# Kernel optimization log

Measured on AMD Instinct MI355X. Metric: run time of the kernel, lower is better.

Reference implementation:

```python
import jax, jax.numpy as jnp
import numpy as np

# ---- fan-beam CT geometry (hard-coded in fidelity_module) ----
N = 256                      # image is N x N on [-20, 20]^2
A = 20                       # number of projection angles over [0, 2pi)
UDET = 624                   # detector pixels on [-60, 60]
S = 768                      # ray samples for line-integral quadrature
R_SRC = 59.0                 # source-to-origin radius
R_DET = 49.0                 # detector-to-origin radius
D_SD = R_SRC + R_DET         # source-to-detector distance
XMIN, XMAX = -20.0, 20.0
DX = (XMAX - XMIN) / N
UMIN, UMAX = -60.0, 60.0
DU = (UMAX - UMIN) / UDET
THETAS = ((np.arange(A) + 0.5) * 2.0 * np.pi / A).astype(np.float32)   # cell midpoints (odl.uniform_partition)
UCENT = (UMIN + (np.arange(UDET) + 0.5) * DU).astype(np.float32)       # detector cell midpoints
NFFT = 2048                  # FFT length for ramp filtering (>= 2*UDET)


def _bilinear(img, gx, gy):
    """img: [B,N,N] (axis0=x, axis1=y). gx, gy: fractional index coords, shape [...].
    Returns [B, ...] with zero outside the image."""
    i0 = jnp.floor(gx)
    j0 = jnp.floor(gy)
    fx = (gx - i0).astype(img.dtype)
    fy = (gy - j0).astype(img.dtype)
    i0 = i0.astype(jnp.int32)
    j0 = j0.astype(jnp.int32)

    def corner(ii, jj):
        valid = (ii >= 0) & (ii < N) & (jj >= 0) & (jj < N)
        v = img[:, jnp.clip(ii, 0, N - 1), jnp.clip(jj, 0, N - 1)]
        return jnp.where(valid[None], v, 0.0)

    return (corner(i0, j0) * (1 - fx) * (1 - fy)
            + corner(i0 + 1, j0) * fx * (1 - fy)
            + corner(i0, j0 + 1) * (1 - fx) * fy
            + corner(i0 + 1, j0 + 1) * fx * fy)


def forward_project(img):
    """Ray-driven fan-beam forward projection (Radon transform). img: [B,N,N] -> sino [B,A,UDET]."""
    cs = jnp.cos(jnp.asarray(THETAS))
    sn = jnp.sin(jnp.asarray(THETAS))
    src = R_SRC * jnp.stack([cs, sn], axis=-1)            # (A,2) source positions
    det_c = -R_DET * jnp.stack([cs, sn], axis=-1)         # (A,2) detector centers
    ddir = jnp.stack([-sn, cs], axis=-1)                  # (A,2) detector axis
    u = jnp.asarray(UCENT)
    p = det_c[:, None, :] + u[None, :, None] * ddir[:, None, :]   # (A,U,2) detector pixel positions
    ray = p - src[:, None, :]                             # (A,U,2)
    length = jnp.sqrt(jnp.sum(ray * ray, axis=-1))        # (A,U) ray length
    tt = (jnp.arange(S, dtype=jnp.float32) + 0.5) / S     # (S,) midpoint quadrature
    pts = src[:, None, None, :] + tt[None, None, :, None] * ray[:, :, None, :]  # (A,U,S,2)
    gx = (pts[..., 0] - XMIN) / DX - 0.5                  # fractional index along axis0 (x)
    gy = (pts[..., 1] - XMIN) / DX - 0.5                  # fractional index along axis1 (y)
    vals = _bilinear(img, gx, gy)                         # (B,A,U,S)
    return jnp.sum(vals, axis=-1) * (length / S)[None]    # (B,A,U)


def fbp(sino):
    """Filtered back-projection with Hann-windowed ramp filter (frequency_scaling=1).
    sino: [B,A,UDET] -> image [B,N,N]."""
    u = jnp.asarray(UCENT)
    # cosine pre-weighting for flat fan-beam detector
    g = sino * (D_SD / jnp.sqrt(D_SD * D_SD + u * u))[None, None, :]
    freqs = jnp.fft.rfftfreq(NFFT, d=DU).astype(jnp.float32)
    nyq = 1.0 / (2.0 * DU)
    ramp = jnp.abs(freqs)
    hann = 0.5 * (1.0 + jnp.cos(np.float32(np.pi) * freqs / nyq)) * (freqs <= nyq)
    filt = ramp * hann
    q = jnp.fft.irfft(jnp.fft.rfft(g, n=NFFT, axis=-1) * filt[None, None, :], n=NFFT, axis=-1)
    q = q[..., :UDET] * DU                                # (B,A,U) filtered sinogram

    cs = jnp.cos(jnp.asarray(THETAS))
    sn = jnp.sin(jnp.asarray(THETAS))
    xs = XMIN + (jnp.arange(N, dtype=jnp.float32) + 0.5) * DX
    X = xs[:, None]                                       # axis0 = x
    Y = xs[None, :]                                       # axis1 = y
    # distance from source plane to pixel along central ray: in [R_SRC-28, R_SRC+28], never ~0
    tdist = R_SRC - (X[None] * cs[:, None, None] + Y[None] * sn[:, None, None])   # (A,N,N)
    uu = D_SD * (-X[None] * sn[:, None, None] + Y[None] * cs[:, None, None]) / tdist  # detector coord of pixel
    k = (uu - UCENT[0]) / DU                              # fractional detector index (A,N,N)
    k0 = jnp.floor(k)
    fk = (k - k0).astype(sino.dtype)
    k0 = k0.astype(jnp.int32)
    aidx = jnp.arange(A)[:, None, None]

    def gather(kk):
        valid = (kk >= 0) & (kk < UDET)
        v = q[:, aidx, jnp.clip(kk, 0, UDET - 1)]         # (B,A,N,N)
        return jnp.where(valid[None], v, 0.0)

    val = gather(k0) * (1 - fk)[None] + gather(k0 + 1) * fk[None]
    w = (R_SRC / tdist) ** 2                              # fan-beam distance weighting
    dtheta = 2.0 * np.pi / A
    return 0.5 * np.float32(dtheta) * jnp.sum(w[None] * val, axis=1)  # (B,N,N)


def setup_inputs() -> dict:
    key = jax.random.key(0)
    k1, k2 = jax.random.split(key)
    input_data = jax.random.uniform(k1, (4, N, N), dtype=jnp.float32)
    proj = jax.random.normal(k2, (4, A, UDET), dtype=jnp.float32)
    return {"input_data": input_data, "proj": proj}


def reference(input_data, proj):
    # fidelity_module.forward: x_error = FBP(proj - Radon(input_data))
    p_tmp = forward_project(input_data)
    y_error = proj - p_tmp
    return fbp(y_error)
```

## Files before the change

### kernel.cpp

```cpp
#include <hip/hip_runtime.h>
#include <math.h>

#define NN 256
#define AA 20
#define UD 624
#define SS 768
#define NAU (AA*UD)
#define PI_D 3.14159265358979323846

__global__ __launch_bounds__(256) void k_prep(const float* __restrict__ img,
                                              float4* __restrict__ pixA,
                                              float4* __restrict__ pixB,
                                              float* __restrict__ hh) {
    __shared__ double red[256];
    const int blk = blockIdx.x;
    const int tid = threadIdx.x;
    if (blk < 256) {
        int idx = blk * 256 + tid;
        float4 v;
        v.x = img[idx];
        v.y = img[65536 + idx];
        v.z = img[131072 + idx];
        v.w = img[196608 + idx];
        pixA[idx] = v;
    } else if (blk < 512) {
        int oidx = (blk - 256) * 256 + tid;
        int j = oidx >> 8, i = oidx & 255;
        int idx = i * 256 + j;
        float4 v;
        v.x = img[idx];
        v.y = img[65536 + idx];
        v.z = img[131072 + idx];
        v.w = img[196608 + idx];
        pixB[oidx] = v;
    } else {
        const int n = blk - 512;
        double acc = 0.0;
        for (int k = 1 + tid; k < 1024; k += 256) {
            float a1 = 1.0f + cosf((float)PI_D * (float)k * (1.0f/1024.0f));
            int m = (k * n) & 2047;
            float c2 = cosf((float)PI_D * (float)m * (1.0f/1024.0f));
            acc += (double)((float)k * a1 * c2);
        }
        red[tid] = acc;
        __syncthreads();
        for (int s = 128; s > 0; s >>= 1) {
            if (tid < s) red[tid] += red[tid + s];
            __syncthreads();
        }
        if (tid == 0) hh[n] = (float)(red[0] * (1.0 / (2048.0 * 2048.0)));
    }
}

__global__ __launch_bounds__(256) void k_forward(const float4* __restrict__ pixA,
                                                 const float4* __restrict__ pixB,
                                                 const float* __restrict__ proj,
                                                 float* __restrict__ g) {
    const int wid = threadIdx.x >> 6;
    const int lane = threadIdx.x & 63;
    const int ray = blockIdx.x * 4 + wid;
    const int a = ray / UD;
    const int u = ray - a * UD;

    const float theta = (float)(((double)a + 0.5) * (2.0 * PI_D / (double)AA));
    float sn, cs;
    sincosf(theta, &sn, &cs);
    const float uc = (float)(-60.0 + ((double)u + 0.5) * (120.0 / 624.0));

    const float sx = 59.0f * cs, sy = 59.0f * sn;
    const float rx = -108.0f * cs - uc * sn;
    const float ry = -108.0f * sn + uc * cs;
    const float length = sqrtf(rx * rx + ry * ry);

    const float stepx = rx * (6.4f / 768.0f);
    const float basex = (sx + rx * (0.5f / 768.0f) + 20.0f) * 6.4f - 0.5f;
    const float stepy = ry * (6.4f / 768.0f);
    const float basey = (sy + ry * (0.5f / 768.0f) + 20.0f) * 6.4f - 0.5f;

    const bool useB = fabsf(stepx) > fabsf(stepy);
    const float4* __restrict__ im = useB ? pixB : pixA;
    const float bi = useB ? basex : basey;
    const float si = useB ? stepx : stepy;
    const float bo = useB ? basey : basex;
    const float so = useB ? stepy : stepx;

    float ax = 0.f, ay = 0.f, az = 0.f, aw = 0.f;

    for (int s = lane; s < SS; s += 64) {
        float gi = fmaf((float)s, si, bi);
        float go = fmaf((float)s, so, bo);
        float fgi = floorf(gi), fgo = floorf(go);
        float fi = gi - fgi, fo = go - fgo;
        int i0 = (int)fgi, o0 = (int)fgo;
        int i1 = i0 + 1, o1 = o0 + 1;
        float wi0 = (i0 >= 0 && i0 < NN) ? (1.0f - fi) : 0.0f;
        float wi1 = (i1 >= 0 && i1 < NN) ? fi : 0.0f;
        float wo0 = (o0 >= 0 && o0 < NN) ? (1.0f - fo) : 0.0f;
        float wo1 = (o1 >= 0 && o1 < NN) ? fo : 0.0f;
        int ic0 = min(max(i0, 0), NN - 1), ic1 = min(max(i1, 0), NN - 1);
        int oc0 = min(max(o0, 0), NN - 1), oc1 = min(max(o1, 0), NN - 1);
        const float4 c00 = im[oc0 * NN + ic0];
        const float4 c10 = im[oc0 * NN + ic1];
        const float4 c01 = im[oc1 * NN + ic0];
        const float4 c11 = im[oc1 * NN + ic1];
        float w00 = wi0 * wo0, w10 = wi1 * wo0, w01 = wi0 * wo1, w11 = wi1 * wo1;
        ax += w00 * c00.x + w10 * c10.x + w01 * c01.x + w11 * c11.x;
        ay += w00 * c00.y + w10 * c10.y + w01 * c01.y + w11 * c11.y;
        az += w00 * c00.z + w10 * c10.z + w01 * c01.z + w11 * c11.z;
        aw += w00 * c00.w + w10 * c10.w + w01 * c01.w + w11 * c11.w;
    }

    for (int off = 32; off > 0; off >>= 1) {
        ax += __shfl_down(ax, off);
        ay += __shfl_down(ay, off);
        az += __shfl_down(az, off);
        aw += __shfl_down(aw, off);
    }

    if (lane == 0) {
        const float scale = length * (1.0f / 768.0f);
        const float wdet = 108.0f / sqrtf(108.0f * 108.0f + uc * uc);
        g[0 * NAU + ray] = (proj[0 * NAU + ray] - ax * scale) * wdet;
        g[1 * NAU + ray] = (proj[1 * NAU + ray] - ay * scale) * wdet;
        g[2 * NAU + ray] = (proj[2 * NAU + ray] - az * scale) * wdet;
        g[3 * NAU + ray] = (proj[3 * NAU + ray] - aw * scale) * wdet;
    }
}

__global__ __launch_bounds__(128) void k_conv(const float* __restrict__ g,
                                              const float* __restrict__ hh,
                                              float* __restrict__ q) {
    __shared__ float sgp[752];
    const int row = blockIdx.x / 5;
    const int tile = blockIdx.x % 5;
    const int tid = threadIdx.x;

    for (int k = tid; k < 752; k += 128) {
        sgp[k] = (k >= 64 && k < 64 + UD) ? g[row * UD + (k - 64)] : 0.0f;
    }
    __syncthreads();

    const int j = tile * 128 + tid;
    const int jc = min(j, UD - 1);
    int wbase = tile * 128 + (tid & 64);
    wbase = __builtin_amdgcn_readfirstlane(wbase);
    const int tmax1 = min(wbase + 63, UD - 1);
    const int tmax2 = UD - 1 - wbase;

    float acc = 0.0f;
    for (int t = 0; t <= tmax1; ++t)
        acc += hh[t] * sgp[64 + jc - t];
    for (int t = 1; t <= tmax2; ++t)
        acc += hh[t] * sgp[64 + jc + t];

    if (j < UD) q[row * UD + j] = acc;
}

__global__ __launch_bounds__(256) void k_bp(const float* __restrict__ q,
                                            float* __restrict__ out) {
    __shared__ float scs[AA], ssn[AA];
    const int tid = threadIdx.x;
    if (tid < AA) {
        float th = (float)(((double)tid + 0.5) * (2.0 * PI_D / (double)AA));
        float s, c;
        sincosf(th, &s, &c);
        scs[tid] = c;
        ssn[tid] = s;
    }
    __syncthreads();

    const int p = blockIdx.x * 256 + tid;
    const int b = p >> 16;
    const int rem = p & 65535;
    const int i = rem >> 8;
    const int j = rem & 255;

    const float X = -20.0f + ((float)i + 0.5f) * 0.15625f;
    const float Y = -20.0f + ((float)j + 0.5f) * 0.15625f;

    const float uc0 = (float)(-60.0 + 0.5 * (120.0 / 624.0));
    const float duf = (float)(120.0 / 624.0);

    const float* __restrict__ qb = q + b * AA * UD;
    float acc = 0.0f;
#pragma unroll
    for (int a = 0; a < AA; ++a) {
        float cs = scs[a], sn = ssn[a];
        float t = 59.0f - (X * cs + Y * sn);
        float uu = 108.0f * (Y * cs - X * sn) / t;
        float k = (uu - uc0) / duf;
        float fk0 = floorf(k);
        float fk = k - fk0;
        int ik = (int)fk0;
        const float* qr = qb + a * UD;
        float v0 = ((unsigned)ik < (unsigned)UD) ? qr[ik] : 0.0f;
        float v1 = ((unsigned)(ik + 1) < (unsigned)UD) ? qr[ik + 1] : 0.0f;
        float val = v0 * (1.0f - fk) + v1 * fk;
        float w = 59.0f / t;
        acc += w * w * val;
    }
    out[p] = (0.5f * (float)(2.0 * PI_D / (double)AA)) * acc;
}

extern "C" void kernel_launch(void* const* d_in, const int* in_sizes, int n_in,
                              void* d_out, int out_size, void* d_ws, size_t ws_size,
                              hipStream_t stream) {
    const float* img  = (const float*)d_in[0];
    const float* proj = (const float*)d_in[1];
    float* out = (float*)d_out;

    char* ws = (char*)d_ws;
    float4* pixA = (float4*)ws;
    float4* pixB = (float4*)(ws + (1 << 20));
    float*  g    = (float*)(ws + (2 << 20));
    float*  q    = (float*)(ws + (2 << 20) + 199680);
    float*  hh   = (float*)(ws + (2 << 20) + 2 * 199680);

    k_prep<<<1136, 256, 0, stream>>>(img, pixA, pixB, hh);
    k_forward<<<NAU / 4, 256, 0, stream>>>(pixA, pixB, proj, g);
    k_conv<<<80 * 5, 128, 0, stream>>>(g, hh, q);
    k_bp<<<1024, 256, 0, stream>>>(q, out);
}
```

Baseline: 114.3 us.

## Pack four rays per wavefront in forward projection and split conv taps across waves

The forward projector now gives each wavefront four adjacent detector rays, with 16 lanes per ray looping over 48 sample steps. This cuts the grid to 780 blocks and shortens the shuffle reduction. Adjacent rays sample nearby pixels, which should improve cache locality. The convolution kernel now spreads each output's tap range over four waves of 256 threads and sums the partials through shared memory, which raises parallelism for the long serial dot products.

After: 116.1 us. No clear change (+1.6%).

```diff
diff --git a/kernel.cpp b/kernel.cpp
--- a/kernel.cpp
+++ b/kernel.cpp
@@ -18,20 +18,14 @@
     if (blk < 256) {
         int idx = blk * 256 + tid;
         float4 v;
-        v.x = img[idx];
-        v.y = img[65536 + idx];
-        v.z = img[131072 + idx];
-        v.w = img[196608 + idx];
+        v.x = img[idx]; v.y = img[65536 + idx]; v.z = img[131072 + idx]; v.w = img[196608 + idx];
         pixA[idx] = v;
     } else if (blk < 512) {
         int oidx = (blk - 256) * 256 + tid;
         int j = oidx >> 8, i = oidx & 255;
         int idx = i * 256 + j;
         float4 v;
-        v.x = img[idx];
-        v.y = img[65536 + idx];
-        v.z = img[131072 + idx];
-        v.w = img[196608 + idx];
+        v.x = img[idx]; v.y = img[65536 + idx]; v.z = img[131072 + idx]; v.w = img[196608 + idx];
         pixB[oidx] = v;
     } else {
         const int n = blk - 512;
@@ -52,20 +46,22 @@
     }
 }
 
-__global__ __launch_bounds__(256) void k_forward(const float4* __restrict__ pixA,
-                                                 const float4* __restrict__ pixB,
-                                                 const float* __restrict__ proj,
-                                                 float* __restrict__ g) {
-    const int wid = threadIdx.x >> 6;
+__global__ __launch_bounds__(256) void k_fwd(const float4* __restrict__ pixA,
+                                             const float4* __restrict__ pixB,
+                                             const float* __restrict__ proj,
+                                             float* __restrict__ g) {
+    const int widx = threadIdx.x >> 6;
     const int lane = threadIdx.x & 63;
-    const int ray = blockIdx.x * 4 + wid;
-    const int a = ray / UD;
-    const int u = ray - a * UD;
+    const int qd = blockIdx.x * 4 + widx;
+    const int a = qd / 156;
+    const int ub = (qd - a * 156) * 4;
+    const int grp = lane >> 4;
+    const int sl = lane & 15;
 
     const float theta = (float)(((double)a + 0.5) * (2.0 * PI_D / (double)AA));
     float sn, cs;
     sincosf(theta, &sn, &cs);
-    const float uc = (float)(-60.0 + ((double)u + 0.5) * (120.0 / 624.0));
+    const float uc = (float)(-60.0 + ((double)(ub + grp) + 0.5) * (120.0 / 624.0));
 
     const float sx = 59.0f * cs, sy = 59.0f * sn;
     const float rx = -108.0f * cs - uc * sn;
@@ -86,7 +82,8 @@
 
     float ax = 0.f, ay = 0.f, az = 0.f, aw = 0.f;
 
-    for (int s = lane; s < SS; s += 64) {
+    for (int it = 0; it < 48; ++it) {
+        const int s = (it << 4) + sl;
         float gi = fmaf((float)s, si, bi);
         float go = fmaf((float)s, so, bo);
         float fgi = floorf(gi), fgo = floorf(go);
@@ -110,14 +107,15 @@
         aw += w00 * c00.w + w10 * c10.w + w01 * c01.w + w11 * c11.w;
     }
 
-    for (int off = 32; off > 0; off >>= 1) {
+    for (int off = 8; off > 0; off >>= 1) {
         ax += __shfl_down(ax, off);
         ay += __shfl_down(ay, off);
         az += __shfl_down(az, off);
         aw += __shfl_down(aw, off);
     }
 
-    if (lane == 0) {
+    if (sl == 0) {
+        const int ray = a * UD + ub + grp;
         const float scale = length * (1.0f / 768.0f);
         const float wdet = 108.0f / sqrtf(108.0f * 108.0f + uc * uc);
         g[0 * NAU + ray] = (proj[0 * NAU + ray] - ax * scale) * wdet;
@@ -127,33 +125,41 @@
     }
 }
 
-__global__ __launch_bounds__(128) void k_conv(const float* __restrict__ g,
+__global__ __launch_bounds__(256) void k_conv(const float* __restrict__ g,
                                               const float* __restrict__ hh,
                                               float* __restrict__ q) {
     __shared__ float sgp[752];
-    const int row = blockIdx.x / 5;
-    const int tile = blockIdx.x % 5;
+    __shared__ float sacc[256];
+    const int row = blockIdx.x / 10;
+    const int jt = blockIdx.x - row * 10;
     const int tid = threadIdx.x;
 
-    for (int k = tid; k < 752; k += 128) {
+    for (int k = tid; k < 752; k += 256)
         sgp[k] = (k >= 64 && k < 64 + UD) ? g[row * UD + (k - 64)] : 0.0f;
-    }
     __syncthreads();
 
-    const int j = tile * 128 + tid;
+    const int jloc = tid & 63;
+    const int seg = tid >> 6;
+    const int j = jt * 64 + jloc;
     const int jc = min(j, UD - 1);
-    int wbase = tile * 128 + (tid & 64);
-    wbase = __builtin_amdgcn_readfirstlane(wbase);
-    const int tmax1 = min(wbase + 63, UD - 1);
-    const int tmax2 = UD - 1 - wbase;
+    const int n1 = min(jt * 64 + 64, UD);
+    const int n2 = UD - 1 - jt * 64;
 
     float acc = 0.0f;
-    for (int t = 0; t <= tmax1; ++t)
-        acc += hh[t] * sgp[64 + jc - t];
-    for (int t = 1; t <= tmax2; ++t)
-        acc += hh[t] * sgp[64 + jc + t];
-
-    if (j < UD) q[row * UD + j] = acc;
+    int t0 = (n1 * seg) >> 2, t1 = (n1 * (seg + 1)) >> 2;
+    for (int t = t0; t < t1; ++t) acc += hh[t] * sgp[64 + jc - t];
+    t0 = 1 + ((n2 * seg) >> 2); t1 = 1 + ((n2 * (seg + 1)) >> 2);
+    for (int t = t0; t < t1; ++t) acc += hh[t] * sgp[64 + jc + t];
+
+    sacc[tid] = acc;
+    __syncthreads();
+    if (tid < 64) {
+        int jj = jt * 64 + tid;
+        if (jj < UD) {
+            float s = sacc[tid] + sacc[64 + tid] + sacc[128 + tid] + sacc[192 + tid];
+            q[row * UD + jj] = s;
+        }
+    }
 }
 
 __global__ __launch_bounds__(256) void k_bp(const float* __restrict__ q,
@@ -213,11 +219,11 @@
     float4* pixA = (float4*)ws;
     float4* pixB = (float4*)(ws + (1 << 20));
     float*  g    = (float*)(ws + (2 << 20));
-    float*  q    = (float*)(ws + (2 << 20) + 199680);
-    float*  hh   = (float*)(ws + (2 << 20) + 2 * 199680);
+    float*  q    = (float*)(ws + (2 << 20) + 200704);
+    float*  hh   = (float*)(ws + (2 << 20) + 401408);
 
     k_prep<<<1136, 256, 0, stream>>>(img, pixA, pixB, hh);
-    k_forward<<<NAU / 4, 256, 0, stream>>>(pixA, pixB, proj, g);
-    k_conv<<<80 * 5, 128, 0, stream>>>(g, hh, q);
-    k_bp<<<1024, 256, 0, stream>>>(q, out);
-}
+    k_fwd <<<780,  256, 0, stream>>>(pixA, pixB, proj, g);
+    k_conv<<<800,  256, 0, stream>>>(g, hh, q);
+    k_bp  <<<1024, 256, 0, stream>>>(q, out);
+}
```
